# Kernel optimization log

Measured on AMD Instinct MI355X. Metric: run time of the kernel, lower is better.

## Reference

```python
import jax, jax.numpy as jnp
import numpy as np

HEADS = 16


def _rope(t):
    # t: [B, H, S, hd]. lucidrains RotaryEmbedding(dim=hd//2): rotates first hd//2
    # channels with interleaved pairs, theta=10000; remaining channels pass through.
    hd = t.shape[-1]
    rot = hd // 2
    S = t.shape[-2]
    inv_freq = 1.0 / (10000.0 ** (jnp.arange(0, rot, 2, dtype=jnp.float32) / rot))  # [rot//2]
    ang = jnp.arange(S, dtype=jnp.float32)[:, None] * inv_freq[None, :]             # [S, rot//2]
    ang = jnp.repeat(ang, 2, axis=-1)                                               # [S, rot]
    cos, sin = jnp.cos(ang), jnp.sin(ang)
    tl, tr = t[..., :rot], t[..., rot:]
    p = tl.reshape(*tl.shape[:-1], rot // 2, 2)
    rh = jnp.stack([-p[..., 1], p[..., 0]], axis=-1).reshape(tl.shape)              # rotate_half
    tl = tl * cos + rh * sin
    return jnp.concatenate([tl, tr], axis=-1)


def setup_inputs() -> dict:
    key = jax.random.key(0)
    ks = jax.random.split(key, 3)
    D = 1024
    return {
        "x": jax.random.normal(ks[0], (2, 2048, D), dtype=jnp.float32),
        "w_qkv": jax.random.normal(ks[1], (D, 3 * D), dtype=jnp.float32) * 0.02,
        "b_qkv": jnp.zeros((3 * D,), dtype=jnp.float32),
        "w_out": jax.random.normal(ks[2], (D, D), dtype=jnp.float32) * 0.02,
        "b_out": jnp.zeros((D,), dtype=jnp.float32),
        "ln_gamma": jnp.ones((D,), dtype=jnp.float32),
        "ln_beta": jnp.zeros((D,), dtype=jnp.float32),
    }


def reference(x, w_qkv, b_qkv, w_out, b_out, ln_gamma, ln_beta):
    B, S, D = x.shape
    hd = D // HEADS
    xp = x @ w_qkv + b_qkv                      # [B, S, 3D]
    q, k, v = jnp.split(xp, 3, axis=-1)
    to_heads = lambda t: t.reshape(B, S, HEADS, hd).transpose(0, 2, 1, 3)  # [B,H,S,hd]
    q, k, v = to_heads(q), to_heads(k), to_heads(v)
    q, k = _rope(q), _rope(k)
    attn = jnp.einsum('bhid,bhjd->bhij', q, k) * (D ** -0.5)  # note: scaled by full h_dim
    attn = jax.nn.softmax(attn, axis=-1)
    xv = jnp.einsum('bhij,bhjd->bhid', attn, v)
    y = xv.transpose(0, 2, 1, 3).reshape(B, S, D) + x         # residual
    y = y @ w_out + b_out
    mu = jnp.mean(y, axis=-1, keepdims=True)
    var = jnp.var(y, axis=-1, keepdims=True)
    y = (y - mu) / jnp.sqrt(var + 1e-5)
    return y * ln_gamma + ln_beta
```

## Files before the change

### kernel.cpp

```cpp
#include <hip/hip_runtime.h>
#include <hip/hip_bf16.h>
#include <math.h>

#define HEADS 16
#define HD 64
#define ROT 32
#define DM 1024
#define N3 3072
#define BB 2
#define SS 2048
#define MM 4096

typedef short short8 __attribute__((ext_vector_type(8)));
typedef float f32x4 __attribute__((ext_vector_type(4)));

__device__ __forceinline__ unsigned int pack2_bf16(float a, float b) {
    __hip_bfloat162 h = __float22bfloat162_rn(make_float2(a, b));
    unsigned int r;
    __builtin_memcpy(&r, &h, 4);
    return r;
}

__device__ __forceinline__ void gload_lds16(const void* g, void* l) {
    __builtin_amdgcn_global_load_lds(
        (const __attribute__((address_space(1))) unsigned int*)g,
        (__attribute__((address_space(3))) unsigned int*)l, 16, 0, 0);
}

__global__ __launch_bounds__(256) void conv_x(
    const float* __restrict__ x, __hip_bfloat16* __restrict__ xb)
{
    int idx = blockIdx.x * 256 + threadIdx.x;
    const float4* src = (const float4*)x;
    float4 v0 = src[idx * 2], v1 = src[idx * 2 + 1];
    uint4 o;
    o.x = pack2_bf16(v0.x, v0.y);
    o.y = pack2_bf16(v0.z, v0.w);
    o.z = pack2_bf16(v1.x, v1.y);
    o.w = pack2_bf16(v1.z, v1.w);
    ((uint4*)xb)[idx] = o;
}

__global__ __launch_bounds__(256) void tr_cast(
    const float* __restrict__ src, __hip_bfloat16* __restrict__ dst,
    int R, int C)
{
    __shared__ float t[32][33];
    const int tx = threadIdx.x, ty = threadIdx.y;
    const int c0 = blockIdx.x * 32, r0 = blockIdx.y * 32;
    #pragma unroll
    for (int k = 0; k < 4; ++k)
        t[ty + k * 8][tx] = src[(size_t)(r0 + ty + k * 8) * C + c0 + tx];
    __syncthreads();
    #pragma unroll
    for (int k = 0; k < 4; ++k)
        dst[(size_t)(c0 + ty + k * 8) * R + r0 + tx] =
            __float2bfloat16(t[tx][ty + k * 8]);
}

__global__ __launch_bounds__(256) void gemm_qkv_mfma(
    const __hip_bfloat16* __restrict__ A, const __hip_bfloat16* __restrict__ Bt,
    const float* __restrict__ bias,
    __hip_bfloat16* __restrict__ Q, __hip_bfloat16* __restrict__ K,
    __hip_bfloat16* __restrict__ Vt)
{
    __shared__ __align__(16) char Asm[8192];
    __shared__ __align__(16) char Bsm[8192];
    const int tid = threadIdx.x;
    const int wid = tid >> 6, lane = tid & 63;
    const int lg = lane >> 4, lc = lane & 15;
    const int wr = wid >> 1, wc = wid & 1;
    const int m0 = blockIdx.x * 128, n0 = blockIdx.y * 128;

    const int idx0 = wid * 128 + lane;
    const int row0 = idx0 >> 2, c16 = idx0 & 3;
    const char* Ag = (const char*)A + (size_t)(m0 + row0) * 2048 + c16 * 16;
    const char* Bg = (const char*)Bt + (size_t)(n0 + row0) * 2048 + c16 * 16;
    char* Al = Asm + wid * 2048;
    char* Bl = Bsm + wid * 2048;

    f32x4 acc[4][4];
    #pragma unroll
    for (int i = 0; i < 4; ++i)
        #pragma unroll
        for (int j = 0; j < 4; ++j) acc[i][j] = f32x4{0.f, 0.f, 0.f, 0.f};

    for (int kb = 0; kb < 2048; kb += 64) {
        if (kb) __syncthreads();
        gload_lds16(Ag + kb, Al);
        gload_lds16(Ag + 32768 + kb, Al + 1024);
        gload_lds16(Bg + kb, Bl);
        gload_lds16(Bg + 32768 + kb, Bl + 1024);
        __syncthreads();

        short8 a[4], b[4];
        #pragma unroll
        for (int mt = 0; mt < 4; ++mt)
            a[mt] = *(const short8*)(Asm + (wr * 64 + mt * 16 + lc) * 64 + lg * 16);
        #pragma unroll
        for (int nt = 0; nt < 4; ++nt)
            b[nt] = *(const short8*)(Bsm + (wc * 64 + nt * 16 + lc) * 64 + lg * 16);
        #pragma unroll
        for (int mt = 0; mt < 4; ++mt)
            #pragma unroll
            for (int nt = 0; nt < 4; ++nt)
                acc[mt][nt] = __builtin_amdgcn_mfma_f32_16x16x32_bf16(
                    a[mt], b[nt], acc[mt][nt], 0, 0, 0);
    }

    #pragma unroll
    for (int nt = 0; nt < 4; ++nt) {
        const int n = n0 + wc * 64 + nt * 16 + lc;
        const int sec = n >> 10;
        const int nd = n & 1023;
        const int h = nd >> 6, d = nd & 63;
        const float bv = bias[n];
        if (sec == 2) {
            #pragma unroll
            for (int mt = 0; mt < 4; ++mt) {
                const int mbase = m0 + wr * 64 + mt * 16 + lg * 4;
                const int s = mbase & (SS - 1);
                const int b = mbase >> 11;
                uint2 pk;
                pk.x = pack2_bf16(acc[mt][nt][0] + bv, acc[mt][nt][1] + bv);
                pk.y = pack2_bf16(acc[mt][nt][2] + bv, acc[mt][nt][3] + bv);
                *(uint2*)((char*)Vt +
                    (((size_t)(b * HEADS + h) * HD + d) * SS + s) * 2) = pk;
            }
        } else {
            const bool rope = (d < ROT);
            const float inv = exp2f(-0.8304820237f * (float)(d >> 1));
            __hip_bfloat16* dst = (sec == 0) ? Q : K;
            const float qs = (sec == 0) ? 0.03125f : 1.0f;
            #pragma unroll
            for (int mt = 0; mt < 4; ++mt) {
                const int mbase = m0 + wr * 64 + mt * 16 + lg * 4;
                #pragma unroll
                for (int reg = 0; reg < 4; ++reg) {
                    const int m = mbase + reg;
                    const int s = m & (SS - 1);
                    const int b = m >> 11;
                    float v = acc[mt][nt][reg] + bv;
                    float partner = __shfl_xor(v, 1);
                    if (rope) {
                        float ang = (float)s * inv;
                        float cs = __cosf(ang), sn = __sinf(ang);
                        v = (lc & 1) ? (v * cs + partner * sn)
                                     : (v * cs - partner * sn);
                    }
                    v *= qs;
                    size_t o = (((size_t)(b * HEADS + h)) * SS + s) * HD + d;
                    dst[o] = __float2bfloat16(v);
                }
            }
        }
    }
}

__global__ __launch_bounds__(256) void attn_mfma(
    const __hip_bfloat16* __restrict__ Qb, const __hip_bfloat16* __restrict__ Kb,
    const __hip_bfloat16* __restrict__ Vtb, const float* __restrict__ x,
    __hip_bfloat16* __restrict__ Y1)
{
    __shared__ __align__(16) char Ksm[8192];
    __shared__ __align__(16) char Vsm[8192];
    __shared__ __align__(16) char Psm[10240];

    const int tid = threadIdx.x;
    const int wid = tid >> 6, lane = tid & 63;
    const int lg = lane >> 4, lc = lane & 15;
    const int bh = blockIdx.y;
    const int b = bh >> 4, h = bh & 15;
    const int q0 = blockIdx.x * 64;

    const int qrow = q0 + wid * 16 + lc;
    const char* qbase = (const char*)(Qb + ((size_t)bh * SS + qrow) * HD);
    short8 qf[2];
    qf[0] = *(const short8*)(qbase + lg * 16);
    qf[1] = *(const short8*)(qbase + 64 + lg * 16);

    f32x4 oacc[4];
    #pragma unroll
    for (int dt = 0; dt < 4; ++dt) oacc[dt] = f32x4{0.f, 0.f, 0.f, 0.f};
    float mrow[4] = {-1e30f, -1e30f, -1e30f, -1e30f};
    float lrow[4] = {0.f, 0.f, 0.f, 0.f};

    const int off0 = wid * 2048 + lane * 16;
    const int off1 = off0 + 1024;
    const int r0 = off0 >> 7, blk0 = (off0 >> 4) & 7;
    const int r1 = off1 >> 7, blk1 = (off1 >> 4) & 7;
    const int sw0 = (blk0 ^ (r0 & 7)) << 4;
    const int sw1 = (blk1 ^ (r1 & 7)) << 4;
    const int ksrc0 = r0 * 128 + sw0;
    const int ksrc1 = r1 * 128 + sw1;
    const int vsrc0 = r0 * (SS * 2) + sw0;
    const int vsrc1 = r1 * (SS * 2) + sw1;
    char* ksl = Ksm + wid * 2048;
    char* vsl = Vsm + wid * 2048;
    char* Pw  = Psm + wid * 2560;

    const char* Kt  = (const char*)(Kb  + (size_t)bh * SS * HD);
    const char* Vtt = (const char*)(Vtb + (size_t)bh * SS * HD);

    for (int kt = 0; kt < SS / 64; ++kt) {
        if (kt) __syncthreads();
        const char* kg = Kt + (size_t)kt * 8192;
        const char* vg = Vtt + (size_t)kt * 128;
        gload_lds16(kg + ksrc0, ksl);
        gload_lds16(kg + ksrc1, ksl + 1024);
        gload_lds16(vg + vsrc0, vsl);
        gload_lds16(vg + vsrc1, vsl + 1024);
        __syncthreads();

        f32x4 sacc[4];
        #pragma unroll
        for (int nt = 0; nt < 4; ++nt) sacc[nt] = f32x4{0.f, 0.f, 0.f, 0.f};
        #pragma unroll
        for (int nt = 0; nt < 4; ++nt) {
            #pragma unroll
            for (int t = 0; t < 2; ++t) {
                int row = nt * 16 + lc;
                int cb = t * 64 + lg * 16;
                short8 kf = *(const short8*)(Ksm + row * 128 + (cb ^ ((row & 7) << 4)));
                sacc[nt] = __builtin_amdgcn_mfma_f32_16x16x32_bf16(qf[t], kf, sacc[nt], 0, 0, 0);
            }
        }

        float mnew[4], corr[4];
        #pragma unroll
        for (int r = 0; r < 4; ++r) {
            float mx = fmaxf(fmaxf(sacc[0][r], sacc[1][r]), fmaxf(sacc[2][r], sacc[3][r]));
            mx = fmaxf(mx, __shfl_xor(mx, 1));
            mx = fmaxf(mx, __shfl_xor(mx, 2));
            mx = fmaxf(mx, __shfl_xor(mx, 4));
            mx = fmaxf(mx, __shfl_xor(mx, 8));
            mnew[r] = fmaxf(mrow[r], mx);
            corr[r] = __expf(mrow[r] - mnew[r]);
            mrow[r] = mnew[r];
        }
        float psum[4] = {0.f, 0.f, 0.f, 0.f};
        #pragma unroll
        for (int nt = 0; nt < 4; ++nt) {
            float p0 = __expf(sacc[nt][0] - mnew[0]);
            float p1 = __expf(sacc[nt][1] - mnew[1]);
            float p2 = __expf(sacc[nt][2] - mnew[2]);
            float p3 = __expf(sacc[nt][3] - mnew[3]);
            psum[0] += p0; psum[1] += p1; psum[2] += p2; psum[3] += p3;
            uint2 w2;
            w2.x = pack2_bf16(p0, p1);
            w2.y = pack2_bf16(p2, p3);
            *(uint2*)(Pw + (nt * 16 + lc) * 40 + lg * 8) = w2;
        }
        #pragma unroll
        for (int r = 0; r < 4; ++r) {
            float s = psum[r];
            s += __shfl_xor(s, 1);
            s += __shfl_xor(s, 2);
            s += __shfl_xor(s, 4);
            s += __shfl_xor(s, 8);
            lrow[r] = lrow[r] * corr[r] + s;
        }
        #pragma unroll
        for (int dt = 0; dt < 4; ++dt) {
            oacc[dt][0] *= corr[0];
            oacc[dt][1] *= corr[1];
            oacc[dt][2] *= corr[2];
            oacc[dt][3] *= corr[3];
        }

        short8 pf[2];
        #pragma unroll
        for (int t = 0; t < 2; ++t)
            #pragma unroll
            for (int j = 0; j < 8; ++j)
                pf[t][j] = *(const short*)(Pw + (t * 32 + lg * 8 + j) * 40 + lc * 2);
        #pragma unroll
        for (int dt = 0; dt < 4; ++dt) {
            #pragma unroll
            for (int t = 0; t < 2; ++t) {
                int vrow = dt * 16 + lc;
                int vcb = t * 64 + lg * 16;
                short8 vf = *(const short8*)(Vsm + vrow * 128 + (vcb ^ ((vrow & 7) << 4)));
                oacc[dt] = __builtin_amdgcn_mfma_f32_16x16x32_bf16(pf[t], vf, oacc[dt], 0, 0, 0);
            }
        }
    }

    #pragma unroll
    for (int r = 0; r < 4; ++r) {
        float inv = 1.0f / lrow[r];
        int qr = q0 + wid * 16 + lg * 4 + r;
        size_t rowoff = ((size_t)b * SS + qr) * DM + h * HD;
        #pragma unroll
        for (int dt = 0; dt < 4; ++dt) {
            int d = dt * 16 + lc;
            Y1[rowoff + d] = __float2bfloat16(oacc[dt][r] * inv + x[rowoff + d]);
        }
    }
}

__global__ __launch_bounds__(256) void gemm_out_mfma(
    const __hip_bfloat16* __restrict__ A, const __hip_bfloat16* __restrict__ Bt,
    const float* __restrict__ bias, float* __restrict__ out)
{
    __shared__ __align__(16) char Asm[8192];
    __shared__ __align__(16) char Bsm[8192];
    const int tid = threadIdx.x;
    const int wid = tid >> 6, lane = tid & 63;
    const int lg = lane >> 4, lc = lane & 15;
    const int wr = wid >> 1, wc = wid & 1;
    const int m0 = blockIdx.x * 128, n0 = blockIdx.y * 128;

    const int idx0 = wid * 128 + lane;
    const int row0 = idx0 >> 2, c16 = idx0 & 3;
    const char* Ag = (const char*)A + (size_t)(m0 + row0) * 2048 + c16 * 16;
    const char* Bg = (const char*)Bt + (size_t)(n0 + row0) * 2048 + c16 * 16;
    char* Al = Asm + wid * 2048;
    char* Bl = Bsm + wid * 2048;

    f32x4 acc[4][4];
    #pragma unroll
    for (int i = 0; i < 4; ++i)
        #pragma unroll
        for (int j = 0; j < 4; ++j) acc[i][j] = f32x4{0.f, 0.f, 0.f, 0.f};

    for (int kb = 0; kb < 2048; kb += 64) {
        if (kb) __syncthreads();
        gload_lds16(Ag + kb, Al);
        gload_lds16(Ag + 32768 + kb, Al + 1024);
        gload_lds16(Bg + kb, Bl);
        gload_lds16(Bg + 32768 + kb, Bl + 1024);
        __syncthreads();

        short8 a[4], b[4];
        #pragma unroll
        for (int mt = 0; mt < 4; ++mt)
            a[mt] = *(const short8*)(Asm + (wr * 64 + mt * 16 + lc) * 64 + lg * 16);
        #pragma unroll
        for (int nt = 0; nt < 4; ++nt)
            b[nt] = *(const short8*)(Bsm + (wc * 64 + nt * 16 + lc) * 64 + lg * 16);
        #pragma unroll
        for (int mt = 0; mt < 4; ++mt)
            #pragma unroll
            for (int nt = 0; nt < 4; ++nt)
                acc[mt][nt] = __builtin_amdgcn_mfma_f32_16x16x32_bf16(
                    a[mt], b[nt], acc[mt][nt], 0, 0, 0);
    }

    #pragma unroll
    for (int nt = 0; nt < 4; ++nt) {
        const int n = n0 + wc * 64 + nt * 16 + lc;
        const float bv = bias[n];
        #pragma unroll
        for (int mt = 0; mt < 4; ++mt) {
            const int mbase = m0 + wr * 64 + mt * 16 + lg * 4;
            #pragma unroll
            for (int reg = 0; reg < 4; ++reg)
                out[(size_t)(mbase + reg) * DM + n] = acc[mt][nt][reg] + bv;
        }
    }
}

__global__ __launch_bounds__(256) void lnorm(
    float* __restrict__ y, const float* __restrict__ gamma,
    const float* __restrict__ beta)
{
    const int row = blockIdx.x;
    const int t = threadIdx.x;
    float* rp = y + (size_t)row * DM;
    float4 v = reinterpret_cast<float4*>(rp)[t];

    float s  = v.x + v.y + v.z + v.w;
    float ss = v.x * v.x + v.y * v.y + v.z * v.z + v.w * v.w;
    #pragma unroll
    for (int off = 32; off > 0; off >>= 1) {
        s  += __shfl_down(s, off);
        ss += __shfl_down(ss, off);
    }
    __shared__ float red[8];
    const int wid = t >> 6;
    if ((t & 63) == 0) { red[wid] = s; red[4 + wid] = ss; }
    __syncthreads();
    if (t == 0) {
        float S   = red[0] + red[1] + red[2] + red[3];
        float SSq = red[4] + red[5] + red[6] + red[7];
        float mu = S / (float)DM;
        red[0] = mu;
        red[4] = SSq / (float)DM - mu * mu;
    }
    __syncthreads();
    const float mu = red[0];
    const float rstd = rsqrtf(red[4] + 1e-5f);

    float4 g  = reinterpret_cast<const float4*>(gamma)[t];
    float4 be = reinterpret_cast<const float4*>(beta)[t];
    float4 o;
    o.x = (v.x - mu) * rstd * g.x + be.x;
    o.y = (v.y - mu) * rstd * g.y + be.y;
    o.z = (v.z - mu) * rstd * g.z + be.z;
    o.w = (v.w - mu) * rstd * g.w + be.w;
    reinterpret_cast<float4*>(rp)[t] = o;
}

extern "C" void kernel_launch(void* const* d_in, const int* in_sizes, int n_in,
                              void* d_out, int out_size, void* d_ws, size_t ws_size,
                              hipStream_t stream)
{
    const float* x      = (const float*)d_in[0];
    const float* w_qkv  = (const float*)d_in[1];
    const float* b_qkv  = (const float*)d_in[2];
    const float* w_out  = (const float*)d_in[3];
    const float* b_out  = (const float*)d_in[4];
    const float* gamma  = (const float*)d_in[5];
    const float* beta   = (const float*)d_in[6];
    float* out = (float*)d_out;
    char* wsb  = (char*)d_ws;

    __hip_bfloat16* xb  = (__hip_bfloat16*)(wsb);
    __hip_bfloat16* wqt = (__hip_bfloat16*)(wsb + (8u << 20));
    __hip_bfloat16* wot = (__hip_bfloat16*)(wsb + (14u << 20));
    __hip_bfloat16* Q   = (__hip_bfloat16*)(wsb + (16u << 20));
    __hip_bfloat16* K   = (__hip_bfloat16*)(wsb + (24u << 20));
    __hip_bfloat16* Vt  = (__hip_bfloat16*)(wsb + (32u << 20));
    __hip_bfloat16* Y1b = (__hip_bfloat16*)(wsb + (40u << 20));

    conv_x<<<2048, 256, 0, stream>>>(x, xb);
    tr_cast<<<dim3(N3 / 32, DM / 32), dim3(32, 8), 0, stream>>>(w_qkv, wqt, DM, N3);
    tr_cast<<<dim3(DM / 32, DM / 32), dim3(32, 8), 0, stream>>>(w_out, wot, DM, DM);

    dim3 g1(MM / 128, N3 / 128);
    gemm_qkv_mfma<<<g1, 256, 0, stream>>>(xb, wqt, b_qkv, Q, K, Vt);

    dim3 g2(SS / 64, BB * HEADS);
    attn_mfma<<<g2, 256, 0, stream>>>(Q, K, Vt, x, Y1b);

    dim3 g3(MM / 128, DM / 128);
    gemm_out_mfma<<<g3, 256, 0, stream>>>(Y1b, wot, b_out, out);

    lnorm<<<MM, 256, 0, stream>>>(out, gamma, beta);
}
```

Measured before the change: 258.8 us.

## Double-buffer K/V tiles in LDS to prefetch the next tile during compute

The attention kernel now keeps two LDS buffers each for K and V. It issues the asynchronous global-to-LDS loads for the next key tile before computing on the current one, and uses a single barrier per iteration instead of two. The goal is to hide global memory latency behind the MFMA and softmax work. The cost is doubled K/V shared memory, roughly 42KB per block instead of 26KB, which may lower occupancy.

```diff
diff --git a/kernel.cpp b/kernel.cpp
--- a/kernel.cpp
+++ b/kernel.cpp
@@ -162,8 +162,8 @@
     const __hip_bfloat16* __restrict__ Vtb, const float* __restrict__ x,
     __hip_bfloat16* __restrict__ Y1)
 {
-    __shared__ __align__(16) char Ksm[8192];
-    __shared__ __align__(16) char Vsm[8192];
+    __shared__ __align__(16) char Ksm[16384];
+    __shared__ __align__(16) char Vsm[16384];
     __shared__ __align__(16) char Psm[10240];
 
     const int tid = threadIdx.x;
@@ -195,22 +195,34 @@
     const int ksrc1 = r1 * 128 + sw1;
     const int vsrc0 = r0 * (SS * 2) + sw0;
     const int vsrc1 = r1 * (SS * 2) + sw1;
-    char* ksl = Ksm + wid * 2048;
-    char* vsl = Vsm + wid * 2048;
-    char* Pw  = Psm + wid * 2560;
+    char* Pw = Psm + wid * 2560;
 
     const char* Kt  = (const char*)(Kb  + (size_t)bh * SS * HD);
     const char* Vtt = (const char*)(Vtb + (size_t)bh * SS * HD);
 
+    {
+        const char* kg = Kt;
+        const char* vg = Vtt;
+        gload_lds16(kg + ksrc0, Ksm + off0);
+        gload_lds16(kg + ksrc1, Ksm + off1);
+        gload_lds16(vg + vsrc0, Vsm + off0);
+        gload_lds16(vg + vsrc1, Vsm + off1);
+    }
+    __syncthreads();
+
+    int buf = 0;
     for (int kt = 0; kt < SS / 64; ++kt) {
-        if (kt) __syncthreads();
-        const char* kg = Kt + (size_t)kt * 8192;
-        const char* vg = Vtt + (size_t)kt * 128;
-        gload_lds16(kg + ksrc0, ksl);
-        gload_lds16(kg + ksrc1, ksl + 1024);
-        gload_lds16(vg + vsrc0, vsl);
-        gload_lds16(vg + vsrc1, vsl + 1024);
-        __syncthreads();
+        if (kt + 1 < SS / 64) {
+            const int bo = (buf ^ 1) << 13;
+            const char* kg = Kt + (size_t)(kt + 1) * 8192;
+            const char* vg = Vtt + (size_t)(kt + 1) * 128;
+            gload_lds16(kg + ksrc0, Ksm + bo + off0);
+            gload_lds16(kg + ksrc1, Ksm + bo + off1);
+            gload_lds16(vg + vsrc0, Vsm + bo + off0);
+            gload_lds16(vg + vsrc1, Vsm + bo + off1);
+        }
+        const char* Kc = Ksm + (buf << 13);
+        const char* Vc = Vsm + (buf << 13);
 
         f32x4 sacc[4];
         #pragma unroll
@@ -221,7 +233,7 @@
             for (int t = 0; t < 2; ++t) {
                 int row = nt * 16 + lc;
                 int cb = t * 64 + lg * 16;
-                short8 kf = *(const short8*)(Ksm + row * 128 + (cb ^ ((row & 7) << 4)));
+                short8 kf = *(const short8*)(Kc + row * 128 + (cb ^ ((row & 7) << 4)));
                 sacc[nt] = __builtin_amdgcn_mfma_f32_16x16x32_bf16(qf[t], kf, sacc[nt], 0, 0, 0);
             }
         }
@@ -280,10 +292,13 @@
             for (int t = 0; t < 2; ++t) {
                 int vrow = dt * 16 + lc;
                 int vcb = t * 64 + lg * 16;
-                short8 vf = *(const short8*)(Vsm + vrow * 128 + (vcb ^ ((vrow & 7) << 4)));
+                short8 vf = *(const short8*)(Vc + vrow * 128 + (vcb ^ ((vrow & 7) << 4)));
                 oacc[dt] = __builtin_amdgcn_mfma_f32_16x16x32_bf16(pf[t], vf, oacc[dt], 0, 0, 0);
             }
         }
+
+        __syncthreads();
+        buf ^= 1;
     }
 
     #pragma unroll
```

New measurement: 273.4 us. +5.6%, slower.

## Use exp2 softmax with lazy max rescaling and deferred row-sum reduction

Applied to the files above, without the earlier changes.

Folds log2(e) into the Q scale so the softmax uses exp2f directly. The running max is rescaled only when some lane's block max grows by more than 8 (a wave-wide vote), which skips most shuffle reductions and accumulator rescales. Per-lane partial row sums are reduced across lanes once at the end instead of every tile. The risk is that un-rescaled probabilities can reach up to 2^8, which bounds the accumulator growth and bf16 precision.

```diff
diff --git a/kernel.cpp b/kernel.cpp
--- a/kernel.cpp
+++ b/kernel.cpp
@@ -131,7 +131,7 @@
             const bool rope = (d < ROT);
             const float inv = exp2f(-0.8304820237f * (float)(d >> 1));
             __hip_bfloat16* dst = (sec == 0) ? Q : K;
-            const float qs = (sec == 0) ? 0.03125f : 1.0f;
+            const float qs = (sec == 0) ? 0.04508422f : 1.0f;
             #pragma unroll
             for (int mt = 0; mt < 4; ++mt) {
                 const int mbase = m0 + wr * 64 + mt * 16 + lg * 4;
@@ -182,8 +182,8 @@
     f32x4 oacc[4];
     #pragma unroll
     for (int dt = 0; dt < 4; ++dt) oacc[dt] = f32x4{0.f, 0.f, 0.f, 0.f};
-    float mrow[4] = {-1e30f, -1e30f, -1e30f, -1e30f};
-    float lrow[4] = {0.f, 0.f, 0.f, 0.f};
+    float mrow[4]  = {-1e30f, -1e30f, -1e30f, -1e30f};
+    float plsum[4] = {0.f, 0.f, 0.f, 0.f};
 
     const int off0 = wid * 2048 + lane * 16;
     const int off1 = off0 + 1024;
@@ -226,46 +226,40 @@
             }
         }
 
-        float mnew[4], corr[4];
-        #pragma unroll
-        for (int r = 0; r < 4; ++r) {
-            float mx = fmaxf(fmaxf(sacc[0][r], sacc[1][r]), fmaxf(sacc[2][r], sacc[3][r]));
-            mx = fmaxf(mx, __shfl_xor(mx, 1));
-            mx = fmaxf(mx, __shfl_xor(mx, 2));
-            mx = fmaxf(mx, __shfl_xor(mx, 4));
-            mx = fmaxf(mx, __shfl_xor(mx, 8));
-            mnew[r] = fmaxf(mrow[r], mx);
-            corr[r] = __expf(mrow[r] - mnew[r]);
-            mrow[r] = mnew[r];
-        }
-        float psum[4] = {0.f, 0.f, 0.f, 0.f};
+        float cmax[4];
+        #pragma unroll
+        for (int r = 0; r < 4; ++r)
+            cmax[r] = fmaxf(fmaxf(sacc[0][r], sacc[1][r]),
+                            fmaxf(sacc[2][r], sacc[3][r]));
+        float dgrow = fmaxf(fmaxf(cmax[0] - mrow[0], cmax[1] - mrow[1]),
+                            fmaxf(cmax[2] - mrow[2], cmax[3] - mrow[3]));
+        if (!__all(dgrow <= 8.0f)) {
+            #pragma unroll
+            for (int r = 0; r < 4; ++r) {
+                float mx = cmax[r];
+                mx = fmaxf(mx, __shfl_xor(mx, 1));
+                mx = fmaxf(mx, __shfl_xor(mx, 2));
+                mx = fmaxf(mx, __shfl_xor(mx, 4));
+                mx = fmaxf(mx, __shfl_xor(mx, 8));
+                float mnew = fmaxf(mrow[r], mx);
+                float corr = exp2f(mrow[r] - mnew);
+                mrow[r] = mnew;
+                plsum[r] *= corr;
+                #pragma unroll
+                for (int dt = 0; dt < 4; ++dt) oacc[dt][r] *= corr;
+            }
+        }
         #pragma unroll
         for (int nt = 0; nt < 4; ++nt) {
-            float p0 = __expf(sacc[nt][0] - mnew[0]);
-            float p1 = __expf(sacc[nt][1] - mnew[1]);
-            float p2 = __expf(sacc[nt][2] - mnew[2]);
-            float p3 = __expf(sacc[nt][3] - mnew[3]);
-            psum[0] += p0; psum[1] += p1; psum[2] += p2; psum[3] += p3;
+            float p0 = exp2f(sacc[nt][0] - mrow[0]);
+            float p1 = exp2f(sacc[nt][1] - mrow[1]);
+            float p2 = exp2f(sacc[nt][2] - mrow[2]);
+            float p3 = exp2f(sacc[nt][3] - mrow[3]);
+            plsum[0] += p0; plsum[1] += p1; plsum[2] += p2; plsum[3] += p3;
             uint2 w2;
             w2.x = pack2_bf16(p0, p1);
             w2.y = pack2_bf16(p2, p3);
             *(uint2*)(Pw + (nt * 16 + lc) * 40 + lg * 8) = w2;
-        }
-        #pragma unroll
-        for (int r = 0; r < 4; ++r) {
-            float s = psum[r];
-            s += __shfl_xor(s, 1);
-            s += __shfl_xor(s, 2);
-            s += __shfl_xor(s, 4);
-            s += __shfl_xor(s, 8);
-            lrow[r] = lrow[r] * corr[r] + s;
-        }
-        #pragma unroll
-        for (int dt = 0; dt < 4; ++dt) {
-            oacc[dt][0] *= corr[0];
-            oacc[dt][1] *= corr[1];
-            oacc[dt][2] *= corr[2];
-            oacc[dt][3] *= corr[3];
         }
 
         short8 pf[2];
@@ -288,7 +282,12 @@
 
     #pragma unroll
     for (int r = 0; r < 4; ++r) {
-        float inv = 1.0f / lrow[r];
+        float s = plsum[r];
+        s += __shfl_xor(s, 1);
+        s += __shfl_xor(s, 2);
+        s += __shfl_xor(s, 4);
+        s += __shfl_xor(s, 8);
+        float inv = 1.0f / s;
         int qr = q0 + wid * 16 + lg * 4 + r;
         size_t rowoff = ((size_t)b * SS + qr) * DM + h * HD;
         #pragma unroll
```

New measurement: 237.3 us. 1.09x faster.
